# Kernel optimization log

Hardware: AMD Instinct MI355X
Metric: run time of the kernel (lower is better)

## Reference

```python
import jax, jax.numpy as jnp
import numpy as np

TOP_K = 2


def setup_inputs() -> dict:
    key = jax.random.key(0)
    k0, k1, k2, k3 = jax.random.split(key, 4)
    N, D, O, E = 131072, 512, 512, 16
    H = D // 4  # gate hidden: gate_input_size // 4
    x = jax.random.normal(k0, (N, D), dtype=jnp.float32)
    # gate MLP params (task_bh=0 gate; Linear weights stored as [in, out])
    Wg1 = jax.random.normal(k1, (D, H), dtype=jnp.float32) / np.sqrt(D).astype(np.float32)
    bg1 = jnp.zeros((H,), jnp.float32)
    Wg2 = jax.random.normal(k2, (H, E), dtype=jnp.float32) * 0.02
    bg2 = jnp.zeros((E,), jnp.float32)
    # per-expert Linear(D, O) weights stacked [E, D, O]
    We = jax.random.normal(k3, (E, D, O), dtype=jnp.float32) / np.sqrt(D).astype(np.float32)
    be = jnp.zeros((E, O), jnp.float32)
    return {"x": x, "Wg1": Wg1, "bg1": bg1, "Wg2": Wg2, "bg2": bg2,
            "We": We, "be": be, "task_bh": 0}


def reference(x, Wg1, bg1, Wg2, bg2, We, be, task_bh):
    # --- top_k_gating (noisy_gating=False path) ---
    h = jax.nn.gelu(x @ Wg1 + bg1, approximate=False)  # nn.GELU default is exact erf
    logits = h @ Wg2 + bg2                              # [N, E]
    probs = jax.nn.softmax(logits, axis=1) + 1e-4       # [N, E]
    top_g, top_i = jax.lax.top_k(probs, TOP_K)          # [N, K]
    N, E = probs.shape
    # dense gate matrix: zeros.scatter(1, top_k_indices, top_k_gates)
    gates = jnp.zeros_like(probs).at[jnp.arange(N)[:, None], top_i].set(top_g)
    # --- dispatch / per-expert GEMM / combine ---
    # Equivalent to: gather tokens per expert, expert Linear, scale by gate,
    # scatter-add back. Since gates[n, e] == 0 for unselected experts, the
    # combined output equals sum_e gates[:, e] * (x @ We[e] + be[e]).
    def body(acc, ewb):
        W_e, b_e, g_e = ewb                      # [D,O], [O], [N]
        return acc + g_e[:, None] * (x @ W_e + b_e), None
    init = jnp.zeros((N, We.shape[2]), x.dtype)
    out, _ = jax.lax.scan(body, init, (We, be, gates.T))
    return out
```

## Files before the change

### kernel.cpp

```cpp
#include <hip/hip_runtime.h>
#include <cstdint>
#include <math.h>


#define NTOK 131072
#define DDIM 512

typedef _Float16 f16;
typedef f16   f16x8 __attribute__((ext_vector_type(8)));
typedef float f32x4 __attribute__((ext_vector_type(4)));

__device__ __forceinline__ void load_lds16(const void* g, void* l){
  __builtin_amdgcn_global_load_lds(
      (const __attribute__((address_space(1))) void*)(uintptr_t)g,
      (__attribute__((address_space(3))) void*)(uintptr_t)l, 16, 0, 0);
}

__device__ __forceinline__ f32x4 MFMAH(f16x8 a, f16x8 b, f32x4 c){
  return __builtin_amdgcn_mfma_f32_16x16x32_f16(a, b, c, 0, 0, 0);
}

__device__ __forceinline__ f16x8 readF64h(const char* buf, int r, int q){
  return *(const f16x8*)(buf + r*128 + ((q ^ (r & 7)) << 4));
}
__device__ __forceinline__ f16x8 readF32h(const char* buf, int r, int q){
  return *(const f16x8*)(buf + r*64 + ((q ^ (r & 3)) << 4));
}
__device__ __forceinline__ f16x8 pack8f(const float* fv){
  f16x8 v;
  #pragma unroll
  for (int j=0;j<8;++j) v[j] = (f16)fv[j];
  return v;
}

__global__ void kconv(const float* __restrict__ Wg1, const float* __restrict__ Wg2,
                      f16* __restrict__ W1, char* __restrict__ Wg2f, int* __restrict__ ctrl){
  __shared__ float sh[64*65];
  int bx = blockIdx.x, tid = threadIdx.x;
  if (bx < 16){
    int dt = bx >> 1, ht = bx & 1;
    const float* src = Wg1 + (size_t)dt*64*128 + ht*64;
    #pragma unroll
    for (int it=0; it<16; ++it){ int idx = it*256+tid; int dl = idx>>6, ol = idx&63;
      sh[dl*65+ol] = src[dl*128+ol]; }
    __syncthreads();
    #pragma unroll
    for (int it=0; it<16; ++it){ int idx = it*256+tid; int ol = idx>>6, dl = idx&63;
      W1[(size_t)(ht*64+ol)*512 + dt*64+dl] = (f16)sh[dl*65+ol]; }
  } else {
    int ks = tid >> 6, l = tid & 63;
    int col = l & 15, kb = ks*32 + ((l >> 4) << 3);
    f16x8 v;
    #pragma unroll
    for (int j=0;j<8;++j) v[j] = (f16)Wg2[(kb+j)*16 + col];
    *(f16x8*)(Wg2f + (ks*64+l)*16) = v;
    #pragma unroll
    for (int i = 0; i < 8; ++i) ctrl[tid + i*256] = 0;
  }
}

__global__ __launch_bounds__(256) void kgate(
    const float* __restrict__ x, const f16* __restrict__ W1, const char* __restrict__ Wg2f,
    const float* __restrict__ bg1, const float* __restrict__ bg2,
    const float* __restrict__ We, f16* __restrict__ Wt,
    f16* __restrict__ xbf,
    int2* __restrict__ gate_e, float2* __restrict__ gate_g,
    int* __restrict__ refine_cnt, int* __restrict__ refine_list, int* __restrict__ counts)
{
  __shared__ __align__(16) char sm[76800];
  const int BOFF = 32768;
  const int LOGI = 67584;
  const int HIST = 75776;
  int tid = threadIdx.x, bid = blockIdx.x;
  int lane = tid & 63, w = tid >> 6, wm = w >> 1, wn = w & 1;
  int l15 = lane & 15, l4 = lane >> 4;
  int t0 = bid * 128;
  int ar = tid >> 1, ach = tid & 1;
  const float* xrow = x + (size_t)(t0 + ar) * DDIM;
  char* xbfb = (char*)xbf;
  f32x4 acc[4][4];
  #pragma unroll
  for (int n=0;n<4;++n){
    float bb = bg1[wn*64 + n*16 + l15];
    f32x4 z = {bb, bb, bb, bb};
    #pragma unroll
    for (int m=0;m<4;++m) acc[m][n] = z;
  }
  auto stageA = [&](int ks, char* abuf){
    float fv[32];
    #pragma unroll
    for (int q=0;q<8;++q) *(float4*)&fv[q*4] = *(const float4*)(xrow + ks*64 + ach*32 + q*4);
    f16x8 h0 = pack8f(fv), h1 = pack8f(fv+8), h2 = pack8f(fv+16), h3 = pack8f(fv+24);
    *(f16x8*)(abuf + ar*128 + (((ach*4+0) ^ (ar & 7)) << 4)) = h0;
    *(f16x8*)(abuf + ar*128 + (((ach*4+1) ^ (ar & 7)) << 4)) = h1;
    *(f16x8*)(abuf + ar*128 + (((ach*4+2) ^ (ar & 7)) << 4)) = h2;
    *(f16x8*)(abuf + ar*128 + (((ach*4+3) ^ (ar & 7)) << 4)) = h3;
    if (xbf){
      char* xd = xbfb + (size_t)(t0+ar)*1024 + ks*128 + ach*64;
      *(f16x8*)xd = h0; *(f16x8*)(xd+16) = h1; *(f16x8*)(xd+32) = h2; *(f16x8*)(xd+48) = h3;
    }
  };
  auto stageB = [&](int ks, char* lds){
    const char* gb = (const char*)W1 + ks*128;
    #pragma unroll
    for (int i = 0; i < 4; ++i){
      int lin = i*4096 + tid*16;
      int r = lin >> 7, g = (lin >> 4) & 7;
      load_lds16(gb + r*1024 + ((g ^ (r & 7)) << 4), lds + i*4096 + ((tid >> 6) << 10));
    }
  };
  stageB(0, sm + BOFF); stageA(0, sm);
  for (int ks = 0; ks < 8; ++ks){
    int b = ks & 1;
    asm volatile("s_waitcnt vmcnt(0)" ::: "memory");
    __syncthreads();
    if (ks < 7) stageB(ks+1, sm + BOFF + (b^1)*16384);
    const char* Ab = sm + b*16384;
    const char* Bb = sm + BOFF + b*16384;
    f16x8 ah[4][2], bh[4][2];
    #pragma unroll
    for (int m=0;m<4;++m)
      #pragma unroll
      for (int kf=0;kf<2;++kf) ah[m][kf] = readF64h(Ab, wm*64 + m*16 + l15, kf*4 + l4);
    #pragma unroll
    for (int n=0;n<4;++n)
      #pragma unroll
      for (int kf=0;kf<2;++kf) bh[n][kf] = readF64h(Bb, wn*64 + n*16 + l15, kf*4 + l4);
    #pragma unroll
    for (int m=0;m<4;++m)
      #pragma unroll
      for (int n=0;n<4;++n){
        acc[m][n] = MFMAH(ah[m][0], bh[n][0], acc[m][n]);
        acc[m][n] = MFMAH(ah[m][1], bh[n][1], acc[m][n]);
      }
    if (ks < 7) stageA(ks+1, sm + (b^1)*16384);
  }
  __syncthreads();
  uint4 wgf[4];
  #pragma unroll
  for (int ksq=0; ksq<4; ++ksq) wgf[ksq] = *(const uint4*)(Wg2f + (ksq*64+lane)*16);
  float* hl = (float*)sm;
  #pragma unroll
  for (int m=0;m<4;++m)
    #pragma unroll
    for (int n=0;n<4;++n)
      #pragma unroll
      for (int j=0;j<4;++j){
        int row = wm*64 + m*16 + (l4 << 2) + j;
        int col = wn*64 + n*16 + l15;
        float uv = acc[m][n][j];
        hl[row*132 + col] = 0.5f * uv * (1.0f + erff(uv * 0.70710678118654752f));
      }
  __syncthreads();
  {
    float bb2 = bg2[l15];
    float* ll = (float*)(sm + LOGI);
    #pragma unroll
    for (int sub=0; sub<2; ++sub){
      f32x4 acc2 = {bb2, bb2, bb2, bb2};
      #pragma unroll
      for (int ksq=0; ksq<4; ++ksq){
        const float* hp = (const float*)sm + (w*32 + sub*16 + l15)*132 + ksq*32 + l4*8;
        f16x8 afr;
        #pragma unroll
        for (int j=0;j<8;++j) afr[j] = (f16)hp[j];
        acc2 = MFMAH(afr, *(const f16x8*)&wgf[ksq], acc2);
      }
      #pragma unroll
      for (int j=0;j<4;++j) ll[(w*32 + sub*16 + l4*4 + j)*16 + l15] = acc2[j];
    }
  }
  int* hist = (int*)(sm + HIST);
  hist[tid] = 0;
  __syncthreads();
  if (tid < 128){
    int t = t0 + tid;
    const float* l = (const float*)(sm + LOGI) + tid*16;
    float b1 = -1e30f, b2 = -1e30f, b3 = -1e30f; int e1 = 0, e2 = 0;
    #pragma unroll
    for (int e = 0; e < 16; ++e){
      float v = l[e];
      if (v > b1){ b3 = b2; b2 = b1; e2 = e1; b1 = v; e1 = e; }
      else if (v > b2){ b3 = b2; b2 = v; e2 = e; }
      else if (v > b3){ b3 = v; }
    }
    float s = 0.f;
    #pragma unroll
    for (int e = 0; e < 16; ++e) s += expf(l[e] - b1);
    float inv = 1.f / s;
    gate_e[t] = make_int2(e1, e2);
    gate_g[t] = make_float2(inv + 1e-4f, expf(b2 - b1) * inv + 1e-4f);
    if (b2 - b3 < 1e-3f){
      int pos = atomicAdd(refine_cnt, 1);
      refine_list[pos] = t;
    }
    int pa = min(e1, e2), pb = max(e1, e2);
    atomicAdd(&hist[pa*16 + pb], 1);
  }
  __syncthreads();
  if (hist[tid]) atomicAdd(&counts[tid], hist[tid]);
  __syncthreads();
  {
    float* sh = (float*)sm;
    int e = bid >> 6, dt = (bid >> 3) & 7, ot = bid & 7;
    const float* src = We + (size_t)e*262144 + (size_t)dt*64*512 + ot*64;
    #pragma unroll
    for (int it=0; it<16; ++it){ int idx = it*256+tid; int dl = idx>>6, ol = idx&63;
      sh[dl*65+ol] = src[dl*512+ol]; }
    __syncthreads();
    f16* dst = Wt + (size_t)e*262144 + (size_t)ot*64*512 + dt*64;
    #pragma unroll
    for (int it=0; it<16; ++it){ int idx = it*256+tid; int ol = idx>>6, dl = idx&63;
      dst[(size_t)ol*512+dl] = (f16)sh[dl*65+ol]; }
  }
}

__global__ __launch_bounds__(128) void krefine(
    const float* __restrict__ x, const float* __restrict__ Wg1, const float* __restrict__ bg1,
    const float* __restrict__ Wg2, const float* __restrict__ bg2,
    const int* __restrict__ refine_cnt, const int* __restrict__ refine_list,
    int2* __restrict__ gate_e, float2* __restrict__ gate_g, int* __restrict__ counts)
{
  __shared__ float  xs[512];
  __shared__ double hd[128];
  __shared__ double ld[16];
  int tid = threadIdx.x;
  int rc = *refine_cnt;
  for (int i = blockIdx.x; i < rc; i += gridDim.x){
    __syncthreads();
    int t = refine_list[i];
    *(float4*)(xs + tid*4) = *(const float4*)(x + (size_t)t*DDIM + tid*4);
    __syncthreads();
    double a0=0.0, a1=0.0, a2=0.0, a3=0.0;
    for (int d = 0; d < 512; d += 4){
      a0 += (double)xs[d]   * (double)Wg1[(d)*128 + tid];
      a1 += (double)xs[d+1] * (double)Wg1[(d+1)*128 + tid];
      a2 += (double)xs[d+2] * (double)Wg1[(d+2)*128 + tid];
      a3 += (double)xs[d+3] * (double)Wg1[(d+3)*128 + tid];
    }
    double a = (double)bg1[tid] + ((a0+a1)+(a2+a3));
    hd[tid] = 0.5 * a * (1.0 + erf(a * 0.70710678118654752440));
    __syncthreads();
    if (tid < 16){
      double s0=0.0, s1=0.0;
      for (int k = 0; k < 128; k += 2){
        s0 += hd[k]   * (double)Wg2[(k)*16 + tid];
        s1 += hd[k+1] * (double)Wg2[(k+1)*16 + tid];
      }
      ld[tid] = (double)bg2[tid] + s0 + s1;
    }
    __syncthreads();
    if (tid == 0){
      int2 olde = gate_e[t];
      double b1 = -1e300, b2 = -1e300; int e1 = 0, e2 = 0;
      for (int e = 0; e < 16; ++e){
        double v = ld[e];
        if (v > b1){ b2 = b1; e2 = e1; b1 = v; e1 = e; }
        else if (v > b2){ b2 = v; e2 = e; }
      }
      double s = 0.0;
      for (int e = 0; e < 16; ++e) s += exp(ld[e] - b1);
      double inv = 1.0 / s;
      int oldp = min(olde.x, olde.y)*16 + max(olde.x, olde.y);
      int newp = min(e1, e2)*16 + max(e1, e2);
      if (oldp != newp){ atomicSub(&counts[oldp], 1); atomicAdd(&counts[newp], 1); }
      gate_e[t] = make_int2(e1, e2);
      gate_g[t] = make_float2((float)(inv + 1e-4), (float)(exp(b2 - b1) * inv + 1e-4));
    }
  }
}

__global__ __launch_bounds__(256) void kscatter(
    const int2* __restrict__ gate_e, const float2* __restrict__ gate_g,
    const int* __restrict__ counts,
    int* __restrict__ bases, int* __restrict__ cursors,
    int* __restrict__ tile_pair, int* __restrict__ tile_row0, int* __restrict__ ntiles,
    int* __restrict__ pair_tok, float2* __restrict__ pair_g, int ts)
{
  __shared__ int h[256];
  __shared__ int gb[256];
  __shared__ int bl[257];
  int tid = threadIdx.x;
  h[tid] = 0;
  if (tid < 64){
    int l = tid;
    int4 c = *(const int4*)(counts + l*4);
    int s = c.x + c.y + c.z + c.w;
    int ps = s;
    #pragma unroll
    for (int d = 1; d < 64; d <<= 1){ int v = __shfl_up(ps, d); if (l >= d) ps += v; }
    int ex = ps - s;
    bl[4*l+0] = ex;
    bl[4*l+1] = ex + c.x;
    bl[4*l+2] = ex + c.x + c.y;
    bl[4*l+3] = ex + c.x + c.y + c.z;
    if (l == 63) bl[256] = ex + s;
    if (blockIdx.x == 0){
      *(int4*)(bases + 4*l) = make_int4(bl[4*l], bl[4*l+1], bl[4*l+2], bl[4*l+3]);
      if (l == 63) bases[256] = ex + s;
      int t0 = (c.x + ts-1)/ts, t1 = (c.y + ts-1)/ts, t2 = (c.z + ts-1)/ts, t3 = (c.w + ts-1)/ts;
      int tsum = t0 + t1 + t2 + t3;
      int pt = tsum;
      #pragma unroll
      for (int d = 1; d < 64; d <<= 1){ int v = __shfl_up(pt, d); if (l >= d) pt += v; }
      int ext = pt - tsum;
      if (l == 63) *ntiles = ext + tsum;
      int tb = ext;
      int cc[4] = {c.x, c.y, c.z, c.w};
      #pragma unroll
      for (int j = 0; j < 4; ++j){
        int pp = 4*l + j;
        for (int r = 0; r < cc[j]; r += ts){ tile_pair[tb] = pp; tile_row0[tb] = r; ++tb; }
      }
    }
  }
  __syncthreads();
  int t = blockIdx.x*256 + tid;
  int2 ee = gate_e[t]; float2 gg = gate_g[t];
  int a, b; float ga, gbv;
  if (ee.x < ee.y){ a = ee.x; b = ee.y; ga = gg.x; gbv = gg.y; }
  else            { a = ee.y; b = ee.x; ga = gg.y; gbv = gg.x; }
  int p = a*16 + b;
  int off = atomicAdd(&h[p], 1);
  __syncthreads();
  if (h[tid]) gb[tid] = bl[tid] + atomicAdd(&cursors[tid], h[tid]);
  __syncthreads();
  int slot = gb[p] + off;
  pair_tok[slot] = t;
  pair_g[slot] = make_float2(ga, gbv);
}

#define SB0 __builtin_amdgcn_sched_barrier(0)

__global__ __launch_bounds__(512, 4) void kexpert3(
    const f16* __restrict__ xbf, const f16* __restrict__ Wt, const float* __restrict__ be,
    float* __restrict__ out,
    const int* __restrict__ counts, const int* __restrict__ bases,
    const int* __restrict__ tile_pair, const int* __restrict__ tile_row0, const int* __restrict__ ntiles,
    const int* __restrict__ pair_tok, const float2* __restrict__ pair_g)
{
  __shared__ __align__(16) char sm[76800];
  const int ABASE = 0, BBASE = 49152, LTOK = 73728, LG = 74752;
  int bid = blockIdx.x;
  int tile = ((bid >> 5) << 3) | (bid & 7);
  int nt = (bid >> 3) & 3;
  if (tile >= *ntiles) return;
  int p = tile_pair[tile], row0 = tile_row0[tile];
  int base = bases[p], cnt = counts[p];
  int eA = p >> 4, eB = p & 15;
  int tid = threadIdx.x, lane = tid & 63, w = tid >> 6;
  int wm = w >> 1, wn = w & 1;
  int l15 = lane & 15, l4 = lane >> 4;
  if (tid < 256){
    int rr = row0 + tid; bool v = rr < cnt;
    ((int*)(sm + LTOK))[tid] = v ? pair_tok[base + rr] : -1;
    ((float2*)(sm + LG))[tid] = v ? pair_g[base + rr] : make_float2(0.f, 1.f);
  }
  __syncthreads();

  int rr = tid >> 2;
  int swz = ((tid & 3) ^ (rr & 3)) << 4;
  const char* xb = (const char*)xbf;
  const char* srcA[2];
  #pragma unroll
  for (int i = 0; i < 2; ++i){
    int tk = ((const int*)(sm + LTOK))[i*128 + rr];
    if (tk < 0) tk = 0;
    srcA[i] = xb + (size_t)tk*1024 + swz;
  }
  const char* srcB0 = (const char*)Wt + (size_t)eA*524288 + (size_t)(nt*128 + rr)*1024 + swz;
  long long edelt = ((long long)eB - eA) * 524288;
  int wbase = w*1024;

  auto stA = [&](int t, int bf_){
    if (t >= 32) return;
    int ks = t & 15;
    load_lds16(srcA[0] + ks*64, sm + ABASE + bf_*16384 + wbase);
    load_lds16(srcA[1] + ks*64, sm + ABASE + bf_*16384 + 8192 + wbase);
  };
  auto stB = [&](int t, int bf_){
    if (t >= 32) return;
    int ks = t & 15;
    long long eo = ((t >= 16) ? edelt : 0) + ks*64;
    load_lds16(srcB0 + eo, sm + BBASE + bf_*8192 + wbase);
  };

  f32x4 acc[4][4];
  #pragma unroll
  for (int m = 0; m < 4; ++m)
    #pragma unroll
    for (int n = 0; n < 4; ++n) acc[m][n] = (f32x4){0.f,0.f,0.f,0.f};

  stA(0, 0); stB(0, 0); stA(1, 1); stB(1, 1);
  asm volatile("s_waitcnt vmcnt(3)"); SB0;
  __builtin_amdgcn_s_barrier();

  int bcur = 0, bstg = 2;
  f16x8 af[4], bb[4];
  #pragma unroll 1
  for (int t = 0; t < 32; ++t){
    const char* Ab = sm + ABASE + bcur*16384;
    const char* Bb = sm + BBASE + bcur*8192;
    #pragma unroll
    for (int m = 0; m < 4; ++m) af[m] = readF32h(Ab, wm*64 + m*16 + l15, l4);
    #pragma unroll
    for (int n = 0; n < 4; ++n) bb[n] = readF32h(Bb, wn*64 + n*16 + l15, l4);
    stA(t+2, bstg); stB(t+2, bstg);
    if (t < 30)       { asm volatile("s_waitcnt vmcnt(3)"); SB0; }
    else if (t == 30) { asm volatile("s_waitcnt vmcnt(0)"); SB0; }
    __builtin_amdgcn_s_barrier();
    asm volatile("s_waitcnt lgkmcnt(0)"); SB0;
    __builtin_amdgcn_s_setprio(1);
    #pragma unroll
    for (int m = 0; m < 4; ++m)
      #pragma unroll
      for (int n = 0; n < 4; ++n)
        acc[m][n] = MFMAH(af[m], bb[n], acc[m][n]);
    __builtin_amdgcn_s_setprio(0);
    SB0;
    __builtin_amdgcn_s_barrier();
    if (t == 15){
      #pragma unroll
      for (int m = 0; m < 4; ++m)
        #pragma unroll
        for (int j = 0; j < 4; ++j){
          int row = wm*64 + m*16 + l4*4 + j;
          float2 g2 = ((const float2*)(sm + LG))[row];
          float r_ = g2.x / g2.y;
          #pragma unroll
          for (int n = 0; n < 4; ++n) acc[m][n][j] *= r_;
        }
    }
    bcur = (bcur == 2) ? 0 : bcur + 1;
    bstg = (bstg == 2) ? 0 : bstg + 1;
  }

  float bcA[4], bcB[4];
  #pragma unroll
  for (int n = 0; n < 4; ++n){
    int col = nt*128 + wn*64 + n*16 + l15;
    bcA[n] = be[(size_t)eA*DDIM + col];
    bcB[n] = be[(size_t)eB*DDIM + col];
  }
  #pragma unroll
  for (int m = 0; m < 4; ++m)
    #pragma unroll
    for (int j = 0; j < 4; ++j){
      int row = wm*64 + m*16 + l4*4 + j;
      int tk = ((const int*)(sm + LTOK))[row];
      if (tk >= 0){
        float2 g2 = ((const float2*)(sm + LG))[row];
        float* orow = out + (size_t)tk*DDIM + nt*128 + wn*64;
        #pragma unroll
        for (int n = 0; n < 4; ++n)
          orow[n*16 + l15] = g2.y*acc[m][n][j] + g2.x*bcA[n] + g2.y*bcB[n];
      }
    }
}

__global__ __launch_bounds__(256, 2) void kexpertF(
    const float* __restrict__ x,
    const f16* __restrict__ Wt, const float* __restrict__ be,
    float* __restrict__ out,
    const int* __restrict__ counts, const int* __restrict__ bases,
    const int* __restrict__ tile_pair, const int* __restrict__ tile_row0, const int* __restrict__ ntiles,
    const int* __restrict__ pair_tok, const float2* __restrict__ pair_g)
{
  __shared__ __align__(16) char sm[67072];
  const int ABUF = 0, BBUF = 32768, LTOK = 65536, LGOFF = 66048;
  int tile = blockIdx.x >> 2, nt = blockIdx.x & 3;
  if (tile >= *ntiles) return;
  int p = tile_pair[tile], row0 = tile_row0[tile];
  int base = bases[p], cnt = counts[p];
  int eA = p >> 4, eB = p & 15;
  int tid = threadIdx.x, lane = tid & 63;
  int w = tid >> 6, wm = w >> 1, wn = w & 1;
  if (tid < 128){
    int rr = row0 + tid; bool v = rr < cnt;
    ((int*)(sm + LTOK))[tid] = v ? pair_tok[base + rr] : -1;
    ((float2*)(sm + LGOFF))[tid] = v ? pair_g[base + rr] : make_float2(0.f, 0.f);
  }
  __syncthreads();
  const char* wb = (const char*)Wt;
  int grp = tid >> 3, gch = tid & 7;
  int swz = (gch ^ (grp & 7)) << 4;
  long long edelt = ((long long)eB - (long long)eA) * 524288;
  const char* srcB[4];
  #pragma unroll
  for (int i = 0; i < 4; ++i)
    srcB[i] = wb + (long long)eA*524288 + (size_t)(nt*128 + i*32 + grp)*1024 + swz;
  int arow = tid >> 1, ach = tid & 1;
  int tkr = ((const int*)(sm + LTOK))[arow];
  if (tkr < 0) tkr = 0;
  const float* xrow = x + (size_t)tkr*DDIM + ach*32;
  int ldst = (w << 10);
  #pragma unroll
  for (int i = 0; i < 4; ++i) load_lds16(srcB[i], sm + BBUF + i*4096 + ldst);
  {
    #pragma unroll
    for (int q2 = 0; q2 < 4; ++q2){
      float fv[8];
      *(float4*)&fv[0] = *(const float4*)(xrow + q2*8);
      *(float4*)&fv[4] = *(const float4*)(xrow + q2*8 + 4);
      f16x8 hv = pack8f(fv);
      int g = ach*4 + q2;
      *(f16x8*)(sm + ABUF + arow*128 + ((g ^ (arow & 7)) << 4)) = hv;
    }
  }
  f32x4 acc[4][4], res[4][4];
  #pragma unroll
  for (int m=0;m<4;++m)
    #pragma unroll
    for (int n=0;n<4;++n) acc[m][n] = (f32x4){0.f,0.f,0.f,0.f};
  for (int u = 0; u < 16; ++u){
    int b = u & 1;
    asm volatile("s_waitcnt vmcnt(0)" ::: "memory");
    __syncthreads();
    int un = u + 1;
    f16x8 hv[4];
    if (un < 16){
      int b2 = un & 1;
      long long aoff = (long long)(un & 7) * 128;
      long long boff = aoff + ((un >> 3) ? edelt : 0);
      #pragma unroll
      for (int i = 0; i < 4; ++i)
        load_lds16(srcB[i] + boff, sm + BBUF + b2*16384 + i*4096 + ldst);
      const float* xr = xrow + (un & 7)*64;
      #pragma unroll
      for (int q2 = 0; q2 < 4; ++q2){
        float fv[8];
        *(float4*)&fv[0] = *(const float4*)(xr + q2*8);
        *(float4*)&fv[4] = *(const float4*)(xr + q2*8 + 4);
        hv[q2] = pack8f(fv);
      }
    }
    const char* Ab = sm + ABUF + b*16384;
    const char* Bb = sm + BBUF + b*16384;
    f16x8 af2[4][2], bf2[4][2];
    #pragma unroll
    for (int m=0;m<4;++m){
      int r = wm*64 + m*16 + (lane & 15);
      af2[m][0] = readF64h(Ab, r, (lane >> 4));
      af2[m][1] = readF64h(Ab, r, 4 + (lane >> 4));
    }
    #pragma unroll
    for (int n=0;n<4;++n){
      int r = wn*64 + n*16 + (lane & 15);
      bf2[n][0] = readF64h(Bb, r, (lane >> 4));
      bf2[n][1] = readF64h(Bb, r, 4 + (lane >> 4));
    }
    #pragma unroll
    for (int m=0;m<4;++m)
      #pragma unroll
      for (int n=0;n<4;++n){
        acc[m][n] = MFMAH(af2[m][0], bf2[n][0], acc[m][n]);
        acc[m][n] = MFMAH(af2[m][1], bf2[n][1], acc[m][n]);
      }
    if (un < 16){
      int b2 = un & 1;
      #pragma unroll
      for (int q2 = 0; q2 < 4; ++q2){
        int g = ach*4 + q2;
        *(f16x8*)(sm + ABUF + b2*16384 + arow*128 + ((g ^ (arow & 7)) << 4)) = hv[q2];
      }
    }
    if (u == 7){
      const float* bev = be + (size_t)eA*DDIM + nt*128;
      float bcol[4];
      #pragma unroll
      for (int n=0;n<4;++n) bcol[n] = bev[wn*64 + n*16 + (lane & 15)];
      #pragma unroll
      for (int m=0;m<4;++m)
        #pragma unroll
        for (int j=0;j<4;++j){
          int row = wm*64 + m*16 + ((lane >> 4) << 2) + j;
          float g = ((const float2*)(sm + LGOFF))[row].x;
          #pragma unroll
          for (int n=0;n<4;++n){
            res[m][n][j] = g * (acc[m][n][j] + bcol[n]);
            acc[m][n][j] = 0.f;
          }
        }
    }
    if (u == 15){
      const float* bev = be + (size_t)eB*DDIM + nt*128;
      float bcol[4];
      #pragma unroll
      for (int n=0;n<4;++n) bcol[n] = bev[wn*64 + n*16 + (lane & 15)];
      #pragma unroll
      for (int m=0;m<4;++m)
        #pragma unroll
        for (int j=0;j<4;++j){
          int row = wm*64 + m*16 + ((lane >> 4) << 2) + j;
          int tk = ((const int*)(sm + LTOK))[row];
          float g = ((const float2*)(sm + LGOFF))[row].y;
          if (tk >= 0){
            float* orow = out + (size_t)tk*DDIM + nt*128;
            #pragma unroll
            for (int n=0;n<4;++n)
              orow[wn*64 + n*16 + (lane & 15)] = res[m][n][j] + g * (acc[m][n][j] + bcol[n]);
          }
        }
    }
  }
}

extern "C" void kernel_launch(void* const* d_in, const int* in_sizes, int n_in,
                              void* d_out, int out_size, void* d_ws, size_t ws_size,
                              hipStream_t stream)
{
  const float* x   = (const float*)d_in[0];
  const float* Wg1 = (const float*)d_in[1];
  const float* bg1 = (const float*)d_in[2];
  const float* Wg2 = (const float*)d_in[3];
  const float* bg2 = (const float*)d_in[4];
  const float* We  = (const float*)d_in[5];
  const float* be  = (const float*)d_in[6];
  float* out = (float*)d_out;
  char* ws = (char*)d_ws;

  f16*  Wt          = (f16*)(ws + 0);
  f16*  W1          = (f16*)(ws + 8388608);
  char* Wg2f        = ws + 8519680;
  char* CTRL        = ws + 8650752;
  int*  refine_cnt  = (int*)(CTRL);
  int*  ntiles      = (int*)(CTRL + 4);
  int*  counts      = (int*)(CTRL + 64);
  int*  cursors     = (int*)(CTRL + 2048);
  int*  bases       = (int*)(CTRL + 4096);
  int2*   gate_e    = (int2*)(ws + 8658944);
  float2* gate_g    = (float2*)(ws + 9707520);
  int*  refine_list = (int*)(ws + 10756096);
  int*  pair_tok    = (int*)(ws + 11280384);
  float2* pair_g    = (float2*)(ws + 11804672);
  int*  tile_pair   = (int*)(ws + 12853248);
  int*  tile_row0   = (int*)(ws + 12863488);
  const size_t XBF_OFF = 16777216ull;
  const size_t XBF_BYTES = (size_t)NTOK * DDIM * 2;
  bool bf16a = ws_size >= XBF_OFF + XBF_BYTES;
  f16* xbf = bf16a ? (f16*)(ws + XBF_OFF) : nullptr;

  hipLaunchKernelGGL(kconv,    dim3(17),   dim3(256), 0, stream, Wg1, Wg2, W1, Wg2f,
                     (int*)CTRL);
  hipLaunchKernelGGL(kgate,    dim3(1024), dim3(256), 0, stream, x, W1, Wg2f, bg1, bg2,
                     We, Wt, xbf, gate_e, gate_g, refine_cnt, refine_list, counts);
  hipLaunchKernelGGL(krefine,  dim3(512),  dim3(128), 0, stream, x, Wg1, bg1, Wg2, bg2,
                     refine_cnt, refine_list, gate_e, gate_g, counts);
  hipLaunchKernelGGL(kscatter, dim3(512),  dim3(256), 0, stream, gate_e, gate_g, counts,
                     bases, cursors, tile_pair, tile_row0, ntiles, pair_tok, pair_g,
                     bf16a ? 256 : 128);
  if (bf16a)
    hipLaunchKernelGGL(kexpert3, dim3(2816), dim3(512), 0, stream, xbf, Wt, be, out,
                       counts, bases, tile_pair, tile_row0, ntiles, pair_tok, pair_g);
  else
    hipLaunchKernelGGL(kexpertF, dim3(5120), dim3(256), 0, stream, x, Wt, be, out,
                       counts, bases, tile_pair, tile_row0, ntiles, pair_tok, pair_g);
  (void)in_sizes; (void)n_in; (void)out_size; (void)ws_size;
}
```

Measured before the change: 468.6 us.

## Repack expert GEMM LDS tiles into 128-byte paired-row swizzled lines

Changes the LDS layout of the expert GEMM A/B stage buffers so two 64-byte rows share one 128-byte line with an XOR-by-line swizzle. The global-to-LDS load addresses are remapped to match, and A and B for each stage sit in one contiguous 24KB region. The aim is fewer LDS bank conflicts on the MFMA operand reads. Separately, the gate-ambiguity threshold for the refinement pass is tightened, which refines fewer tokens, and the refine grid is doubled. Both cut refine work but could change which expert is picked when scores are near-ties.

```diff
diff --git a/kernel.cpp b/kernel.cpp
--- a/kernel.cpp
+++ b/kernel.cpp
@@ -23,8 +23,10 @@
 __device__ __forceinline__ f16x8 readF64h(const char* buf, int r, int q){
   return *(const f16x8*)(buf + r*128 + ((q ^ (r & 7)) << 4));
 }
-__device__ __forceinline__ f16x8 readF32h(const char* buf, int r, int q){
-  return *(const f16x8*)(buf + r*64 + ((q ^ (r & 3)) << 4));
+__device__ __forceinline__ f16x8 readP32(const char* buf, int r, int q){
+  int line = r >> 1;
+  int slot = (((r & 1) << 2) | q) ^ (line & 7);
+  return *(const f16x8*)(buf + line*128 + (slot << 4));
 }
 __device__ __forceinline__ f16x8 pack8f(const float* fv){
   f16x8 v;
@@ -190,7 +192,7 @@
     float inv = 1.f / s;
     gate_e[t] = make_int2(e1, e2);
     gate_g[t] = make_float2(inv + 1e-4f, expf(b2 - b1) * inv + 1e-4f);
-    if (b2 - b3 < 1e-3f){
+    if (b2 - b3 < 4e-4f){
       int pos = atomicAdd(refine_cnt, 1);
       refine_list[pos] = t;
     }
@@ -332,7 +334,7 @@
 
 #define SB0 __builtin_amdgcn_sched_barrier(0)
 
-__global__ __launch_bounds__(512, 4) void kexpert3(
+__global__ __launch_bounds__(512, 4) void kexpert4(
     const f16* __restrict__ xbf, const f16* __restrict__ Wt, const float* __restrict__ be,
     float* __restrict__ out,
     const int* __restrict__ counts, const int* __restrict__ bases,
@@ -340,7 +342,7 @@
     const int* __restrict__ pair_tok, const float2* __restrict__ pair_g)
 {
   __shared__ __align__(16) char sm[76800];
-  const int ABASE = 0, BBASE = 49152, LTOK = 73728, LG = 74752;
+  const int LTOK = 73728, LG = 74752;
   int bid = blockIdx.x;
   int tile = ((bid >> 5) << 3) | (bid & 7);
   int nt = (bid >> 3) & 3;
@@ -358,31 +360,40 @@
   }
   __syncthreads();
 
-  int rr = tid >> 2;
-  int swz = ((tid & 3) ^ (rr & 3)) << 4;
   const char* xb = (const char*)xbf;
   const char* srcA[2];
   #pragma unroll
-  for (int i = 0; i < 2; ++i){
-    int tk = ((const int*)(sm + LTOK))[i*128 + rr];
+  for (int c = 0; c < 2; ++c){
+    int slice = w*2 + c;
+    int line = slice*8 + (lane >> 3);
+    int slotp = (lane & 7) ^ (line & 7);
+    int r = (line << 1) | (slotp >> 2);
+    int q = slotp & 3;
+    int tk = ((const int*)(sm + LTOK))[r];
     if (tk < 0) tk = 0;
-    srcA[i] = xb + (size_t)tk*1024 + swz;
-  }
-  const char* srcB0 = (const char*)Wt + (size_t)eA*524288 + (size_t)(nt*128 + rr)*1024 + swz;
+    srcA[c] = xb + (size_t)tk*1024 + q*16;
+  }
+  const char* srcB0;
+  {
+    int line = w*8 + (lane >> 3);
+    int slotp = (lane & 7) ^ (line & 7);
+    int r = (line << 1) | (slotp >> 2);
+    int q = slotp & 3;
+    srcB0 = (const char*)Wt + (size_t)eA*524288 + (size_t)(nt*128 + r)*1024 + q*16;
+  }
   long long edelt = ((long long)eB - eA) * 524288;
-  int wbase = w*1024;
 
   auto stA = [&](int t, int bf_){
     if (t >= 32) return;
     int ks = t & 15;
-    load_lds16(srcA[0] + ks*64, sm + ABASE + bf_*16384 + wbase);
-    load_lds16(srcA[1] + ks*64, sm + ABASE + bf_*16384 + 8192 + wbase);
+    load_lds16(srcA[0] + ks*64, sm + bf_*24576 + (w*2)*1024);
+    load_lds16(srcA[1] + ks*64, sm + bf_*24576 + (w*2+1)*1024);
   };
   auto stB = [&](int t, int bf_){
     if (t >= 32) return;
     int ks = t & 15;
     long long eo = ((t >= 16) ? edelt : 0) + ks*64;
-    load_lds16(srcB0 + eo, sm + BBASE + bf_*8192 + wbase);
+    load_lds16(srcB0 + eo, sm + bf_*24576 + 16384 + w*1024);
   };
 
   f32x4 acc[4][4];
@@ -399,12 +410,12 @@
   f16x8 af[4], bb[4];
   #pragma unroll 1
   for (int t = 0; t < 32; ++t){
-    const char* Ab = sm + ABASE + bcur*16384;
-    const char* Bb = sm + BBASE + bcur*8192;
-    #pragma unroll
-    for (int m = 0; m < 4; ++m) af[m] = readF32h(Ab, wm*64 + m*16 + l15, l4);
-    #pragma unroll
-    for (int n = 0; n < 4; ++n) bb[n] = readF32h(Bb, wn*64 + n*16 + l15, l4);
+    const char* Ab = sm + bcur*24576;
+    const char* Bb = Ab + 16384;
+    #pragma unroll
+    for (int m = 0; m < 4; ++m) af[m] = readP32(Ab, wm*64 + m*16 + l15, l4);
+    #pragma unroll
+    for (int n = 0; n < 4; ++n) bb[n] = readP32(Bb, wn*64 + n*16 + l15, l4);
     stA(t+2, bstg); stB(t+2, bstg);
     if (t < 30)       { asm volatile("s_waitcnt vmcnt(3)"); SB0; }
     else if (t == 30) { asm volatile("s_waitcnt vmcnt(0)"); SB0; }
@@ -644,13 +655,13 @@
                      (int*)CTRL);
   hipLaunchKernelGGL(kgate,    dim3(1024), dim3(256), 0, stream, x, W1, Wg2f, bg1, bg2,
                      We, Wt, xbf, gate_e, gate_g, refine_cnt, refine_list, counts);
-  hipLaunchKernelGGL(krefine,  dim3(512),  dim3(128), 0, stream, x, Wg1, bg1, Wg2, bg2,
+  hipLaunchKernelGGL(krefine,  dim3(1024), dim3(128), 0, stream, x, Wg1, bg1, Wg2, bg2,
                      refine_cnt, refine_list, gate_e, gate_g, counts);
   hipLaunchKernelGGL(kscatter, dim3(512),  dim3(256), 0, stream, gate_e, gate_g, counts,
                      bases, cursors, tile_pair, tile_row0, ntiles, pair_tok, pair_g,
                      bf16a ? 256 : 128);
   if (bf16a)
-    hipLaunchKernelGGL(kexpert3, dim3(2816), dim3(512), 0, stream, xbf, Wt, be, out,
+    hipLaunchKernelGGL(kexpert4, dim3(2816), dim3(512), 0, stream, xbf, Wt, be, out,
                        counts, bases, tile_pair, tile_row0, ntiles, pair_tok, pair_g);
   else
     hipLaunchKernelGGL(kexpertF, dim3(5120), dim3(256), 0, stream, x, Wt, be, out,
```

New measurement: 410.0 us. 1.14x faster.
